# Kernel tuning notes

Measured on AMD Instinct MI355X. Metric: run time of the kernel, lower is better.

## Reference

```python
import jax, jax.numpy as jnp
import numpy as np

N_NODES = 100000
N_EDGES = 1600000
IN_DIM = 256
HID = 32
HEADS = 4
NEG_SLOPE = 0.2


def _seg_softmax(e, seg, n):
    # numerically stable softmax of e [E, H] over segments (destination nodes)
    m = jax.ops.segment_max(e, seg, num_segments=n)
    ex = jnp.exp(e - m[seg])
    s = jax.ops.segment_sum(ex, seg, num_segments=n)
    return ex / (s[seg] + 1e-16)


def _gat_layer(x, W, a_src, a_dst, b, src, dst, n):
    H, D = a_src.shape
    h = (x @ W).reshape(n, H, D)                       # [N, H, D]
    e_src = jnp.sum(h * a_src, axis=-1)                # [N, H]
    e_dst = jnp.sum(h * a_dst, axis=-1)                # [N, H]
    e = jax.nn.leaky_relu(e_src[src] + e_dst[dst], NEG_SLOPE)  # [E, H]
    alpha = _seg_softmax(e, dst, n)                    # [E, H]
    msg = h[src] * alpha[:, :, None]                   # [E, H, D]
    out = jax.ops.segment_sum(msg, dst, num_segments=n)
    return out.reshape(n, H * D) + b


def setup_inputs() -> dict:
    key = jax.random.key(0)
    ks = jax.random.split(key, 20)
    x = jax.random.normal(ks[0], (N_NODES, IN_DIM), dtype=jnp.float32)
    edge_index = jax.random.randint(ks[1], (2, N_EDGES), 0, N_NODES, dtype=jnp.int64)
    s = 0.05
    inp = {"x": x, "edge_index": edge_index}
    inp["W_in"] = jax.random.normal(ks[2], (IN_DIM, HID), dtype=jnp.float32) * s
    inp["b_in"] = jnp.zeros((HID,), dtype=jnp.float32)
    in_dims = [HID, HID * HEADS, HID * HEADS]
    for l in range(3):
        k = jax.random.split(ks[3 + l], 4)
        inp[f"W{l}"] = jax.random.normal(k[0], (in_dims[l], HEADS * HID), dtype=jnp.float32) * s
        inp[f"a_src{l}"] = jax.random.normal(k[1], (HEADS, HID), dtype=jnp.float32) * s
        inp[f"a_dst{l}"] = jax.random.normal(k[2], (HEADS, HID), dtype=jnp.float32) * s
        inp[f"b{l}"] = jnp.zeros((HEADS * HID,), dtype=jnp.float32)
    return inp


def reference(x, edge_index, W_in, b_in,
              W0, a_src0, a_dst0, b0,
              W1, a_src1, a_dst1, b1,
              W2, a_src2, a_dst2, b2):
    n = x.shape[0]
    # PyG GATConv adds self-loops by default
    loops = jnp.arange(n, dtype=edge_index.dtype)
    src = jnp.concatenate([edge_index[0], loops])
    dst = jnp.concatenate([edge_index[1], loops])

    h = jax.nn.relu(x @ W_in + b_in)
    params = [(W0, a_src0, a_dst0, b0), (W1, a_src1, a_dst1, b1), (W2, a_src2, a_dst2, b2)]
    for (W, a_s, a_d, b) in params:
        h = _gat_layer(h, W, a_s, a_d, b, src, dst, n)
        h = jax.nn.elu(h)
        # dropout omitted (eval mode / deterministic reference)
    return h
```

## Files before the change

kernel.cpp:

```cpp
#include <hip/hip_runtime.h>
#include <hip/hip_fp16.h>

#define NN 100000
#define NE 1600000
#define ET (NE + NN)
#define BKW 512
#define NBK ((NN + BKW - 1) / BKW)
#define LCOL_CAP 12288
#define EPB 16384

typedef _Float16 half8_t __attribute__((ext_vector_type(8)));
typedef float f32x4_t __attribute__((ext_vector_type(4)));

__device__ __forceinline__ unsigned enc_f32(float v) {
    unsigned b = __float_as_uint(v);
    return b ^ ((b & 0x80000000u) ? 0xFFFFFFFFu : 0x80000000u);
}
__device__ __forceinline__ float dec_f32(unsigned u) {
    unsigned b = (u & 0x80000000u) ? (u ^ 0x80000000u) : ~u;
    return __uint_as_float(b);
}


__global__ __launch_bounds__(256) void lin_relu2(const float* __restrict__ x,
                                                 const float* __restrict__ W,
                                                 const float* __restrict__ b,
                                                 float* __restrict__ h) {
    __shared__ float Wl[256 * 32];
    int t = threadIdx.x;
    for (int j = 0; j < 8; ++j) {
        int f = t + 256 * j;
        *(float4*)&Wl[f * 4] = *(const float4*)(W + f * 4);
    }
    __syncthreads();

    int row = (blockIdx.x * 256 + t) >> 3;
    int c0  = (t & 7) * 4;
    const float* xr = x + (long long)row * 256;
    float4 acc = {0.f, 0.f, 0.f, 0.f};
    for (int k4 = 0; k4 < 64; ++k4) {
        float4 xv = *(const float4*)(xr + k4 * 4);
        float4 w0 = *(const float4*)&Wl[(k4 * 4 + 0) * 32 + c0];
        float4 w1 = *(const float4*)&Wl[(k4 * 4 + 1) * 32 + c0];
        float4 w2 = *(const float4*)&Wl[(k4 * 4 + 2) * 32 + c0];
        float4 w3 = *(const float4*)&Wl[(k4 * 4 + 3) * 32 + c0];
        acc.x += xv.x * w0.x + xv.y * w1.x + xv.z * w2.x + xv.w * w3.x;
        acc.y += xv.x * w0.y + xv.y * w1.y + xv.z * w2.y + xv.w * w3.y;
        acc.z += xv.x * w0.z + xv.y * w1.z + xv.z * w2.z + xv.w * w3.z;
        acc.w += xv.x * w0.w + xv.y * w1.w + xv.z * w2.w + xv.w * w3.w;
    }
    float4 bv = *(const float4*)(b + c0);
    acc.x = fmaxf(acc.x + bv.x, 0.f);
    acc.y = fmaxf(acc.y + bv.y, 0.f);
    acc.z = fmaxf(acc.z + bv.z, 0.f);
    acc.w = fmaxf(acc.w + bv.w, 0.f);
    *(float4*)(h + (long long)row * 32 + c0) = acc;
}

template<int K>
__global__ __launch_bounds__(256) void gemm_att5(const float* __restrict__ hin,
                                                 const float* __restrict__ W,
                                                 const float* __restrict__ asrc,
                                                 const float* __restrict__ adst,
                                                 __half* __restrict__ hph,
                                                 float* __restrict__ es,
                                                 float* __restrict__ ed,
                                                 unsigned* __restrict__ mxl) {
    __shared__ float hl[64][K + 4];
    __shared__ unsigned lmx[8];
    int t = threadIdx.x;
    int base = blockIdx.x * 64;

    for (int j = 0; j < K / 16; ++j) {
        int f = t + 256 * j;
        int row = f / (K / 4);
        int kq = f % (K / 4);
        int gr = base + row;
        float4 v = {0.f, 0.f, 0.f, 0.f};
        if (gr < NN) v = *(const float4*)(hin + (long long)gr * K + kq * 4);
        *(float4*)&hl[row][kq * 4] = v;
    }
    if (t < 8) lmx[t] = 0u;
    __syncthreads();

    int cg = t & 31, c0 = cg * 4;
    int rq = t >> 5, r0 = rq * 8;
    float4 acc[8];
    #pragma unroll
    for (int i = 0; i < 8; ++i) acc[i] = make_float4(0.f, 0.f, 0.f, 0.f);

    for (int k4 = 0; k4 < K / 4; ++k4) {
        float4 w0 = *(const float4*)(W + (k4 * 4 + 0) * 128 + c0);
        float4 w1 = *(const float4*)(W + (k4 * 4 + 1) * 128 + c0);
        float4 w2 = *(const float4*)(W + (k4 * 4 + 2) * 128 + c0);
        float4 w3 = *(const float4*)(W + (k4 * 4 + 3) * 128 + c0);
        #pragma unroll
        for (int i = 0; i < 8; ++i) {
            float4 hv = *(const float4*)&hl[r0 + i][k4 * 4];
            acc[i].x += hv.x * w0.x + hv.y * w1.x + hv.z * w2.x + hv.w * w3.x;
            acc[i].y += hv.x * w0.y + hv.y * w1.y + hv.z * w2.y + hv.w * w3.y;
            acc[i].z += hv.x * w0.z + hv.y * w1.z + hv.z * w2.z + hv.w * w3.z;
            acc[i].w += hv.x * w0.w + hv.y * w1.w + hv.z * w2.w + hv.w * w3.w;
        }
    }

    int head = cg >> 3;
    int d0 = (cg & 7) * 4;
    float4 as4 = *(const float4*)(asrc + head * 32 + d0);
    float4 ad4 = *(const float4*)(adst + head * 32 + d0);
    float smax = -1e30f, dmax = -1e30f;
    #pragma unroll
    for (int i = 0; i < 8; ++i) {
        int gr = base + r0 + i;
        if (gr >= NN) break;
        __half2 p0 = __floats2half2_rn(acc[i].x, acc[i].y);
        __half2 p1 = __floats2half2_rn(acc[i].z, acc[i].w);
        uint2 pk;
        pk.x = *(unsigned*)&p0;
        pk.y = *(unsigned*)&p1;
        *(uint2*)(hph + (long long)gr * 128 + c0) = pk;
        float ps = acc[i].x * as4.x + acc[i].y * as4.y + acc[i].z * as4.z + acc[i].w * as4.w;
        float pd = acc[i].x * ad4.x + acc[i].y * ad4.y + acc[i].z * ad4.z + acc[i].w * ad4.w;
        for (int off = 1; off < 8; off <<= 1) {
            ps += __shfl_xor(ps, off, 8);
            pd += __shfl_xor(pd, off, 8);
        }
        if ((cg & 7) == 0) {
            es[gr * 4 + head] = ps;
            ed[gr * 4 + head] = pd;
            smax = fmaxf(smax, ps);
            dmax = fmaxf(dmax, pd);
        }
    }
    if ((cg & 7) == 0) {
        atomicMax(&lmx[head], enc_f32(smax));
        atomicMax(&lmx[4 + head], enc_f32(dmax));
    }
    __syncthreads();
    if (t < 8) atomicMax(mxl + t, lmx[t]);
}

__global__ __launch_bounds__(256) void wf_prep(const float* __restrict__ W,
                                               _Float16* __restrict__ Wf) {
    int id = blockIdx.x * 256 + threadIdx.x;
    if (id >= 2048) return;
    int lane = id & 63;
    int q = id >> 6;
    int ks = q & 3;
    int n = q >> 2;
    int col = n * 16 + (lane & 15);
    int k0 = ks * 32 + ((lane >> 4) << 3);
    _Float16 tmp[8];
    #pragma unroll
    for (int j = 0; j < 8; ++j) tmp[j] = (_Float16)W[(k0 + j) * 128 + col];
    *(half8_t*)(Wf + (size_t)id * 8) = *(half8_t*)tmp;
}

__global__ __launch_bounds__(256) void gemm_mfma(const __half* __restrict__ ah,
                                                 const _Float16* __restrict__ Wf,
                                                 const float* __restrict__ asrc,
                                                 const float* __restrict__ adst,
                                                 __half* __restrict__ hph,
                                                 float* __restrict__ es,
                                                 float* __restrict__ ed,
                                                 unsigned* __restrict__ mxl) {
    __shared__ unsigned lmx[8];
    int t = threadIdx.x;
    if (t < 8) lmx[t] = 0u;
    __syncthreads();

    int lane = t & 63, wid = t >> 6;
    int li = lane & 15, lg = lane >> 4;
    int base = blockIdx.x * 128 + wid * 32;
    int r0 = base + li, r1 = r0 + 16;
    long long r0c = min(r0, NN - 1), r1c = min(r1, NN - 1);
    const _Float16* A = (const _Float16*)ah;

    f32x4_t acc[2][8];
    #pragma unroll
    for (int m = 0; m < 2; ++m)
        #pragma unroll
        for (int n = 0; n < 8; ++n) acc[m][n] = (f32x4_t){0.f, 0.f, 0.f, 0.f};

    #pragma unroll
    for (int ks = 0; ks < 4; ++ks) {
        half8_t a0 = *(const half8_t*)(A + r0c * 128 + ks * 32 + lg * 8);
        half8_t a1 = *(const half8_t*)(A + r1c * 128 + ks * 32 + lg * 8);
        #pragma unroll
        for (int n = 0; n < 8; ++n) {
            half8_t b = *(const half8_t*)(Wf + (size_t)((n * 4 + ks) * 64 + lane) * 8);
            acc[0][n] = __builtin_amdgcn_mfma_f32_16x16x32_f16(a0, b, acc[0][n], 0, 0, 0);
            acc[1][n] = __builtin_amdgcn_mfma_f32_16x16x32_f16(a1, b, acc[1][n], 0, 0, 0);
        }
    }

    float as_lo[4], as_hi[4], ad_lo[4], ad_hi[4];
    #pragma unroll
    for (int h = 0; h < 4; ++h) {
        as_lo[h] = asrc[h * 32 + li];
        as_hi[h] = asrc[h * 32 + 16 + li];
        ad_lo[h] = adst[h * 32 + li];
        ad_hi[h] = adst[h * 32 + 16 + li];
    }

    float smax[4] = {-1e30f, -1e30f, -1e30f, -1e30f};
    float dmax[4] = {-1e30f, -1e30f, -1e30f, -1e30f};
    #pragma unroll
    for (int m = 0; m < 2; ++m) {
        #pragma unroll
        for (int r = 0; r < 4; ++r) {
            int gr = base + m * 16 + lg * 4 + r;
            bool valid = gr < NN;
            float ps[4], pd[4];
            #pragma unroll
            for (int h = 0; h < 4; ++h) {
                float va = acc[m][2 * h][r];
                float vb = acc[m][2 * h + 1][r];
                if (valid) {
                    hph[(long long)gr * 128 + h * 32 + li] = __float2half(va);
                    hph[(long long)gr * 128 + h * 32 + 16 + li] = __float2half(vb);
                }
                ps[h] = va * as_lo[h] + vb * as_hi[h];
                pd[h] = va * ad_lo[h] + vb * ad_hi[h];
            }
            #pragma unroll
            for (int off = 1; off < 16; off <<= 1) {
                #pragma unroll
                for (int h = 0; h < 4; ++h) {
                    ps[h] += __shfl_xor(ps[h], off);
                    pd[h] += __shfl_xor(pd[h], off);
                }
            }
            if (li == 0 && valid) {
                #pragma unroll
                for (int h = 0; h < 4; ++h) {
                    es[gr * 4 + h] = ps[h];
                    ed[gr * 4 + h] = pd[h];
                    smax[h] = fmaxf(smax[h], ps[h]);
                    dmax[h] = fmaxf(dmax[h], pd[h]);
                }
            }
        }
    }
    if (li == 0) {
        #pragma unroll
        for (int h = 0; h < 4; ++h) {
            atomicMax(&lmx[h], enc_f32(smax[h]));
            atomicMax(&lmx[4 + h], enc_f32(dmax[h]));
        }
    }
    __syncthreads();
    if (t < 8) atomicMax(mxl + t, lmx[t]);
}


__global__ __launch_bounds__(256) void bucket_hist(const int* __restrict__ ei,
                                                   int* __restrict__ bhist) {
    __shared__ int lh[NBK];
    int t = threadIdx.x;
    for (int i = t; i < NBK; i += 256) lh[i] = 0;
    __syncthreads();
    for (long long e = (long long)blockIdx.x * 256 + t; e < ET; e += (long long)gridDim.x * 256) {
        int dst = (e < NE) ? ei[NE + e] : (int)(e - NE);
        atomicAdd(&lh[dst >> 9], 1);
    }
    __syncthreads();
    for (int i = t; i < NBK; i += 256) if (lh[i]) atomicAdd(&bhist[i], lh[i]);
}

__global__ __launch_bounds__(256) void bucket_scan(const int* __restrict__ bhist,
                                                   int* __restrict__ bbase,
                                                   int* __restrict__ bcur) {
    __shared__ int ls[256];
    int t = threadIdx.x;
    int v = (t < NBK) ? bhist[t] : 0;
    ls[t] = v;
    __syncthreads();
    for (int off = 1; off < 256; off <<= 1) {
        int u = (t >= off) ? ls[t - off] : 0;
        __syncthreads();
        ls[t] += u;
        __syncthreads();
    }
    if (t < NBK) { int b0 = ls[t] - v; bbase[t] = b0; bcur[t] = b0; }
    if (t == 0) bbase[NBK] = ET;
}

__global__ __launch_bounds__(256) void bucket_scatter(const int* __restrict__ ei,
                                                      int* __restrict__ bcur,
                                                      unsigned* __restrict__ brec) {
    __shared__ int lcnt[NBK];
    __shared__ int lbase[NBK];
    int t = threadIdx.x;
    long long e0 = (long long)blockIdx.x * EPB;
    for (int i = t; i < NBK; i += 256) lcnt[i] = 0;
    __syncthreads();
    for (int j = 0; j < EPB / 256; ++j) {
        long long e = e0 + j * 256 + t;
        if (e < ET) {
            int dst = (e < NE) ? ei[NE + e] : (int)(e - NE);
            atomicAdd(&lcnt[dst >> 9], 1);
        }
    }
    __syncthreads();
    for (int i = t; i < NBK; i += 256) {
        int c = lcnt[i];
        lbase[i] = c ? atomicAdd(&bcur[i], c) : 0;
        lcnt[i] = 0;
    }
    __syncthreads();
    for (int j = 0; j < EPB / 256; ++j) {
        long long e = e0 + j * 256 + t;
        if (e < ET) {
            int src, dst;
            if (e < NE) { src = ei[e]; dst = ei[NE + e]; }
            else        { src = dst = (int)(e - NE); }
            int b = dst >> 9;
            int off = atomicAdd(&lcnt[b], 1);
            brec[lbase[b] + off] = ((unsigned)(dst & 511) << 17) | (unsigned)src;
        }
    }
}

__global__ __launch_bounds__(256) void bucket_csr(const unsigned* __restrict__ brec,
                                                  const int* __restrict__ bbase,
                                                  int* __restrict__ row_ptr,
                                                  int* __restrict__ col) {
    __shared__ int ldeg[BKW];
    __shared__ int lrp[BKW + 1];
    __shared__ int lcur[BKW];
    __shared__ int ls[256];
    __shared__ int lcol[LCOL_CAP];
    int t = threadIdx.x, b = blockIdx.x;
    int rbeg = bbase[b], rend = bbase[b + 1];
    int cnt = rend - rbeg;
    for (int i = t; i < BKW; i += 256) ldeg[i] = 0;
    __syncthreads();
    for (int i = t; i < cnt; i += 256) {
        unsigned r = brec[rbeg + i];
        atomicAdd(&ldeg[r >> 17], 1);
    }
    __syncthreads();
    int a0 = ldeg[2 * t], a1 = ldeg[2 * t + 1];
    int pl = a0 + a1;
    ls[t] = pl;
    __syncthreads();
    for (int off = 1; off < 256; off <<= 1) {
        int u = (t >= off) ? ls[t - off] : 0;
        __syncthreads();
        ls[t] += u;
        __syncthreads();
    }
    int eb = ls[t] - pl;
    lrp[2 * t] = eb;
    lrp[2 * t + 1] = eb + a0;
    lcur[2 * t] = eb;
    lcur[2 * t + 1] = eb + a0;
    if (t == 255) lrp[BKW] = ls[255];
    __syncthreads();
    int gn0 = b * BKW;
    int nnb = min(BKW, NN - gn0);
    for (int i = t; i <= nnb; i += 256) row_ptr[gn0 + i] = rbeg + lrp[i];
    for (int i = t; i < cnt; i += 256) {
        unsigned r = brec[rbeg + i];
        int pos = atomicAdd(&lcur[r >> 17], 1);
        lcol[pos] = (int)(r & 0x1FFFFu);
    }
    __syncthreads();
    for (int i = t; i < cnt; i += 256) col[rbeg + i] = lcol[i];
}

__global__ __launch_bounds__(256) void gat_aggregate4(
        const int* __restrict__ row_ptr, const int* __restrict__ col,
        const float* __restrict__ es, const float* __restrict__ ed,
        const unsigned* __restrict__ mx, const __half* __restrict__ hph,
        const float* __restrict__ b, float* __restrict__ outf,
        __half* __restrict__ outh) {
    int tid = blockIdx.x * 256 + threadIdx.x;
    int n = tid >> 4;
    int t = tid & 15;
    if (n >= NN) return;
    int head = t >> 2;
    int beg = row_ptr[n], end = row_ptr[n + 1];

    float Craw = dec_f32(mx[head]) + dec_f32(mx[4 + head]);
    float C = Craw > 0.f ? Craw : 0.2f * Craw;
    float edv = ed[n * 4 + head];

    float acc[8] = {0.f, 0.f, 0.f, 0.f, 0.f, 0.f, 0.f, 0.f};
    float ws = 0.f;
    const __half* hb = hph + (long long)t * 8;

    int i = beg;
    for (; i + 3 < end; i += 4) {
        int s0 = col[i], s1 = col[i + 1], s2 = col[i + 2], s3 = col[i + 3];
        float l0 = es[s0 * 4 + head] + edv;
        float l1 = es[s1 * 4 + head] + edv;
        float l2 = es[s2 * 4 + head] + edv;
        float l3 = es[s3 * 4 + head] + edv;
        uint4 g0 = *(const uint4*)(hb + (long long)s0 * 128);
        uint4 g1 = *(const uint4*)(hb + (long long)s1 * 128);
        uint4 g2 = *(const uint4*)(hb + (long long)s2 * 128);
        uint4 g3 = *(const uint4*)(hb + (long long)s3 * 128);
        l0 = l0 > 0.f ? l0 : 0.2f * l0;
        l1 = l1 > 0.f ? l1 : 0.2f * l1;
        l2 = l2 > 0.f ? l2 : 0.2f * l2;
        l3 = l3 > 0.f ? l3 : 0.2f * l3;
        float w0 = __expf(l0 - C);
        float w1 = __expf(l1 - C);
        float w2 = __expf(l2 - C);
        float w3 = __expf(l3 - C);
        ws += (w0 + w1) + (w2 + w3);
        float2 f;
        f = __half22float2(*(__half2*)&g0.x); acc[0] += w0 * f.x; acc[1] += w0 * f.y;
        f = __half22float2(*(__half2*)&g0.y); acc[2] += w0 * f.x; acc[3] += w0 * f.y;
        f = __half22float2(*(__half2*)&g0.z); acc[4] += w0 * f.x; acc[5] += w0 * f.y;
        f = __half22float2(*(__half2*)&g0.w); acc[6] += w0 * f.x; acc[7] += w0 * f.y;
        f = __half22float2(*(__half2*)&g1.x); acc[0] += w1 * f.x; acc[1] += w1 * f.y;
        f = __half22float2(*(__half2*)&g1.y); acc[2] += w1 * f.x; acc[3] += w1 * f.y;
        f = __half22float2(*(__half2*)&g1.z); acc[4] += w1 * f.x; acc[5] += w1 * f.y;
        f = __half22float2(*(__half2*)&g1.w); acc[6] += w1 * f.x; acc[7] += w1 * f.y;
        f = __half22float2(*(__half2*)&g2.x); acc[0] += w2 * f.x; acc[1] += w2 * f.y;
        f = __half22float2(*(__half2*)&g2.y); acc[2] += w2 * f.x; acc[3] += w2 * f.y;
        f = __half22float2(*(__half2*)&g2.z); acc[4] += w2 * f.x; acc[5] += w2 * f.y;
        f = __half22float2(*(__half2*)&g2.w); acc[6] += w2 * f.x; acc[7] += w2 * f.y;
        f = __half22float2(*(__half2*)&g3.x); acc[0] += w3 * f.x; acc[1] += w3 * f.y;
        f = __half22float2(*(__half2*)&g3.y); acc[2] += w3 * f.x; acc[3] += w3 * f.y;
        f = __half22float2(*(__half2*)&g3.z); acc[4] += w3 * f.x; acc[5] += w3 * f.y;
        f = __half22float2(*(__half2*)&g3.w); acc[6] += w3 * f.x; acc[7] += w3 * f.y;
    }
    for (; i < end; ++i) {
        int s = col[i];
        float lv = es[s * 4 + head] + edv;
        lv = lv > 0.f ? lv : 0.2f * lv;
        float w = __expf(lv - C);
        ws += w;
        uint4 g = *(const uint4*)(hb + (long long)s * 128);
        float2 f;
        f = __half22float2(*(__half2*)&g.x); acc[0] += w * f.x; acc[1] += w * f.y;
        f = __half22float2(*(__half2*)&g.y); acc[2] += w * f.x; acc[3] += w * f.y;
        f = __half22float2(*(__half2*)&g.z); acc[4] += w * f.x; acc[5] += w * f.y;
        f = __half22float2(*(__half2*)&g.w); acc[6] += w * f.x; acc[7] += w * f.y;
    }
    float sv = ws + 1e-16f;
    float vals[8];
    #pragma unroll
    for (int j = 0; j < 8; ++j) {
        float v = acc[j] / sv + b[t * 8 + j];
        vals[j] = v > 0.f ? v : expm1f(v);
    }
    if (outf) {
        float4 v0 = {vals[0], vals[1], vals[2], vals[3]};
        float4 v1 = {vals[4], vals[5], vals[6], vals[7]};
        *(float4*)(outf + (long long)n * 128 + t * 8) = v0;
        *(float4*)(outf + (long long)n * 128 + t * 8 + 4) = v1;
    } else {
        __half o[8];
        #pragma unroll
        for (int j = 0; j < 8; ++j) o[j] = __float2half(vals[j]);
        *(uint4*)(outh + (long long)n * 128 + t * 8) = *(uint4*)o;
    }
}


extern "C" void kernel_launch(void* const* d_in, const int* in_sizes, int n_in,
                              void* d_out, int out_size, void* d_ws, size_t ws_size,
                              hipStream_t stream) {
    const float* x    = (const float*)d_in[0];
    const int*   ei   = (const int*)d_in[1];
    const float* W_in = (const float*)d_in[2];
    const float* b_in = (const float*)d_in[3];
    const float* W[3]  = {(const float*)d_in[4], (const float*)d_in[8],  (const float*)d_in[12]};
    const float* As[3] = {(const float*)d_in[5], (const float*)d_in[9],  (const float*)d_in[13]};
    const float* Ad[3] = {(const float*)d_in[6], (const float*)d_in[10], (const float*)d_in[14]};
    const float* Bs[3] = {(const float*)d_in[7], (const float*)d_in[11], (const float*)d_in[15]};

    float*    h0   = (float*)d_ws;
    __half*   hph  = (__half*)(h0 + (size_t)NN * 32);
    __half*   ah   = hph + (size_t)NN * 128;
    float*    es   = (float*)(ah + (size_t)NN * 128);
    float*    ed   = es + (size_t)NN * 4;
    int*   row_ptr = (int*)(ed + (size_t)NN * 4);
    int*    bhist  = row_ptr + (NN + 1);
    int*    bbase  = bhist + NBK;
    int*    bcur   = bbase + (NBK + 1);
    unsigned* mx   = (unsigned*)(bcur + NBK);
    _Float16* Wf1  = (_Float16*)(mx + 24);
    _Float16* Wf2  = Wf1 + 2048 * 8;
    unsigned* brec = (unsigned*)(Wf2 + 2048 * 8);
    int*    colb   = (int*)(brec + ET);

    hipMemsetAsync(bhist, 0, NBK * sizeof(int), stream);
    hipMemsetAsync(mx, 0, 24 * sizeof(unsigned), stream);
    bucket_hist<<<512, 256, 0, stream>>>(ei, bhist);
    bucket_scan<<<1, 256, 0, stream>>>(bhist, bbase, bcur);
    bucket_scatter<<<(ET + EPB - 1) / EPB, 256, 0, stream>>>(ei, bcur, brec);
    bucket_csr<<<NBK, 256, 0, stream>>>(brec, bbase, row_ptr, colb);

    lin_relu2<<<3125, 256, 0, stream>>>(x, W_in, b_in, h0);
    wf_prep<<<8, 256, 0, stream>>>(W[1], Wf1);
    wf_prep<<<8, 256, 0, stream>>>(W[2], Wf2);

    gemm_att5<32><<<1563, 256, 0, stream>>>(h0, W[0], As[0], Ad[0], hph, es, ed, mx);
    gat_aggregate4<<<6250, 256, 0, stream>>>(row_ptr, colb, es, ed, mx, hph, Bs[0],
                                             nullptr, ah);
    gemm_mfma<<<782, 256, 0, stream>>>(ah, Wf1, As[1], Ad[1], hph, es, ed, mx + 8);
    gat_aggregate4<<<6250, 256, 0, stream>>>(row_ptr, colb, es, ed, mx + 8, hph, Bs[1],
                                             nullptr, ah);
    gemm_mfma<<<782, 256, 0, stream>>>(ah, Wf2, As[2], Ad[2], hph, es, ed, mx + 16);
    gat_aggregate4<<<6250, 256, 0, stream>>>(row_ptr, colb, es, ed, mx + 16, hph, Bs[2],
                                             (float*)d_out, nullptr);
}
```

Baseline: 499.3 us.

## Sort nodes by degree and share attention weights across lanes in aggregation

Adds a counting sort of destination nodes by in-degree (histogram, scan, scatter), so each wavefront handles nodes of similar degree and divergence in the edge loop shrinks. The aggregation kernel now walks nodes through that permutation, aligns the column index to a multiple of 4 so it can use int4 loads, and has each of the 4 lanes in a head compute one edge's exp weight, then broadcast it with shuffles instead of every lane computing all four. The cost is three small extra kernels and an indirection per node. Output writes become scattered in node order, and the peeling loop adds some extra scalar work.

```diff
diff --git a/kernel.cpp b/kernel.cpp
--- a/kernel.cpp
+++ b/kernel.cpp
@@ -370,17 +370,52 @@
     for (int i = t; i < cnt; i += 256) col[rbeg + i] = lcol[i];
 }
 
-__global__ __launch_bounds__(256) void gat_aggregate4(
+__global__ __launch_bounds__(256) void deg_hist(const int* __restrict__ row_ptr,
+                                                int* __restrict__ dh) {
+    int n = blockIdx.x * 256 + threadIdx.x;
+    if (n >= NN) return;
+    int d = row_ptr[n + 1] - row_ptr[n];
+    atomicAdd(dh + min(d, 63), 1);
+}
+__global__ __launch_bounds__(64) void deg_scan(const int* __restrict__ dh,
+                                               int* __restrict__ dcur) {
+    __shared__ int ls[64];
+    int t = threadIdx.x;
+    int v = dh[t];
+    ls[t] = v;
+    __syncthreads();
+    for (int off = 1; off < 64; off <<= 1) {
+        int u = (t >= off) ? ls[t - off] : 0;
+        __syncthreads();
+        ls[t] += u;
+        __syncthreads();
+    }
+    dcur[t] = ls[t] - v;
+}
+__global__ __launch_bounds__(256) void deg_scatter(const int* __restrict__ row_ptr,
+                                                   int* __restrict__ dcur,
+                                                   int* __restrict__ nperm) {
+    int n = blockIdx.x * 256 + threadIdx.x;
+    if (n >= NN) return;
+    int d = row_ptr[n + 1] - row_ptr[n];
+    int p = atomicAdd(dcur + min(d, 63), 1);
+    nperm[p] = n;
+}
+
+__global__ __launch_bounds__(256) void gat_aggregate5(
+        const int* __restrict__ nperm,
         const int* __restrict__ row_ptr, const int* __restrict__ col,
         const float* __restrict__ es, const float* __restrict__ ed,
         const unsigned* __restrict__ mx, const __half* __restrict__ hph,
         const float* __restrict__ b, float* __restrict__ outf,
         __half* __restrict__ outh) {
     int tid = blockIdx.x * 256 + threadIdx.x;
-    int n = tid >> 4;
+    int g = tid >> 4;
     int t = tid & 15;
-    if (n >= NN) return;
+    if (g >= NN) return;
+    int n = nperm[g];
     int head = t >> 2;
+    int j = t & 3;
     int beg = row_ptr[n], end = row_ptr[n + 1];
 
     float Craw = dec_f32(mx[head]) + dec_f32(mx[4 + head]);
@@ -392,24 +427,34 @@
     const __half* hb = hph + (long long)t * 8;
 
     int i = beg;
+    int alim = (beg + 3) & ~3;
+    for (; i < end && i < alim; ++i) {
+        int s = col[i];
+        float lv = es[s * 4 + head] + edv;
+        lv = lv > 0.f ? lv : 0.2f * lv;
+        float w = __expf(lv - C);
+        ws += w;
+        uint4 gv = *(const uint4*)(hb + (long long)s * 128);
+        float2 f;
+        f = __half22float2(*(__half2*)&gv.x); acc[0] += w * f.x; acc[1] += w * f.y;
+        f = __half22float2(*(__half2*)&gv.y); acc[2] += w * f.x; acc[3] += w * f.y;
+        f = __half22float2(*(__half2*)&gv.z); acc[4] += w * f.x; acc[5] += w * f.y;
+        f = __half22float2(*(__half2*)&gv.w); acc[6] += w * f.x; acc[7] += w * f.y;
+    }
     for (; i + 3 < end; i += 4) {
-        int s0 = col[i], s1 = col[i + 1], s2 = col[i + 2], s3 = col[i + 3];
-        float l0 = es[s0 * 4 + head] + edv;
-        float l1 = es[s1 * 4 + head] + edv;
-        float l2 = es[s2 * 4 + head] + edv;
-        float l3 = es[s3 * 4 + head] + edv;
-        uint4 g0 = *(const uint4*)(hb + (long long)s0 * 128);
-        uint4 g1 = *(const uint4*)(hb + (long long)s1 * 128);
-        uint4 g2 = *(const uint4*)(hb + (long long)s2 * 128);
-        uint4 g3 = *(const uint4*)(hb + (long long)s3 * 128);
-        l0 = l0 > 0.f ? l0 : 0.2f * l0;
-        l1 = l1 > 0.f ? l1 : 0.2f * l1;
-        l2 = l2 > 0.f ? l2 : 0.2f * l2;
-        l3 = l3 > 0.f ? l3 : 0.2f * l3;
-        float w0 = __expf(l0 - C);
-        float w1 = __expf(l1 - C);
-        float w2 = __expf(l2 - C);
-        float w3 = __expf(l3 - C);
+        int4 s4 = *(const int4*)(col + i);
+        int sj = (j == 0) ? s4.x : (j == 1) ? s4.y : (j == 2) ? s4.z : s4.w;
+        float lv = es[sj * 4 + head] + edv;
+        lv = lv > 0.f ? lv : 0.2f * lv;
+        float wj = __expf(lv - C);
+        float w0 = __shfl(wj, 0, 4);
+        float w1 = __shfl(wj, 1, 4);
+        float w2 = __shfl(wj, 2, 4);
+        float w3 = __shfl(wj, 3, 4);
+        uint4 g0 = *(const uint4*)(hb + (long long)s4.x * 128);
+        uint4 g1 = *(const uint4*)(hb + (long long)s4.y * 128);
+        uint4 g2 = *(const uint4*)(hb + (long long)s4.z * 128);
+        uint4 g3 = *(const uint4*)(hb + (long long)s4.w * 128);
         ws += (w0 + w1) + (w2 + w3);
         float2 f;
         f = __half22float2(*(__half2*)&g0.x); acc[0] += w0 * f.x; acc[1] += w0 * f.y;
@@ -435,19 +480,20 @@
         lv = lv > 0.f ? lv : 0.2f * lv;
         float w = __expf(lv - C);
         ws += w;
-        uint4 g = *(const uint4*)(hb + (long long)s * 128);
+        uint4 gv = *(const uint4*)(hb + (long long)s * 128);
         float2 f;
-        f = __half22float2(*(__half2*)&g.x); acc[0] += w * f.x; acc[1] += w * f.y;
-        f = __half22float2(*(__half2*)&g.y); acc[2] += w * f.x; acc[3] += w * f.y;
-        f = __half22float2(*(__half2*)&g.z); acc[4] += w * f.x; acc[5] += w * f.y;
-        f = __half22float2(*(__half2*)&g.w); acc[6] += w * f.x; acc[7] += w * f.y;
-    }
+        f = __half22float2(*(__half2*)&gv.x); acc[0] += w * f.x; acc[1] += w * f.y;
+        f = __half22float2(*(__half2*)&gv.y); acc[2] += w * f.x; acc[3] += w * f.y;
+        f = __half22float2(*(__half2*)&gv.z); acc[4] += w * f.x; acc[5] += w * f.y;
+        f = __half22float2(*(__half2*)&gv.w); acc[6] += w * f.x; acc[7] += w * f.y;
+    }
+
     float sv = ws + 1e-16f;
     float vals[8];
     #pragma unroll
-    for (int j = 0; j < 8; ++j) {
-        float v = acc[j] / sv + b[t * 8 + j];
-        vals[j] = v > 0.f ? v : expm1f(v);
+    for (int k = 0; k < 8; ++k) {
+        float v = acc[k] / sv + b[t * 8 + k];
+        vals[k] = v > 0.f ? v : expm1f(v);
     }
     if (outf) {
         float4 v0 = {vals[0], vals[1], vals[2], vals[3]};
@@ -457,7 +503,7 @@
     } else {
         __half o[8];
         #pragma unroll
-        for (int j = 0; j < 8; ++j) o[j] = __float2half(vals[j]);
+        for (int k = 0; k < 8; ++k) o[k] = __float2half(vals[k]);
         *(uint4*)(outh + (long long)n * 128 + t * 8) = *(uint4*)o;
     }
 }
@@ -485,29 +531,36 @@
     int*    bbase  = bhist + NBK;
     int*    bcur   = bbase + (NBK + 1);
     unsigned* mx   = (unsigned*)(bcur + NBK);
-    _Float16* Wf1  = (_Float16*)(mx + 24);
+    int*    dh     = (int*)(mx + 24);
+    int*    dcur   = dh + 64;
+    int*    nperm  = dcur + 64;
+    _Float16* Wf1  = (_Float16*)(nperm + NN);
     _Float16* Wf2  = Wf1 + 2048 * 8;
     unsigned* brec = (unsigned*)(Wf2 + 2048 * 8);
     int*    colb   = (int*)(brec + ET);
 
     hipMemsetAsync(bhist, 0, NBK * sizeof(int), stream);
     hipMemsetAsync(mx, 0, 24 * sizeof(unsigned), stream);
+    hipMemsetAsync(dh, 0, 64 * sizeof(int), stream);
     bucket_hist<<<512, 256, 0, stream>>>(ei, bhist);
     bucket_scan<<<1, 256, 0, stream>>>(bhist, bbase, bcur);
     bucket_scatter<<<(ET + EPB - 1) / EPB, 256, 0, stream>>>(ei, bcur, brec);
     bucket_csr<<<NBK, 256, 0, stream>>>(brec, bbase, row_ptr, colb);
+    deg_hist<<<(NN + 255) / 256, 256, 0, stream>>>(row_ptr, dh);
+    deg_scan<<<1, 64, 0, stream>>>(dh, dcur);
+    deg_scatter<<<(NN + 255) / 256, 256, 0, stream>>>(row_ptr, dcur, nperm);
 
     lin_relu2<<<3125, 256, 0, stream>>>(x, W_in, b_in, h0);
     wf_prep<<<8, 256, 0, stream>>>(W[1], Wf1);
     wf_prep<<<8, 256, 0, stream>>>(W[2], Wf2);
 
     gemm_att5<32><<<1563, 256, 0, stream>>>(h0, W[0], As[0], Ad[0], hph, es, ed, mx);
-    gat_aggregate4<<<6250, 256, 0, stream>>>(row_ptr, colb, es, ed, mx, hph, Bs[0],
+    gat_aggregate5<<<6250, 256, 0, stream>>>(nperm, row_ptr, colb, es, ed, mx, hph, Bs[0],
                                              nullptr, ah);
     gemm_mfma<<<782, 256, 0, stream>>>(ah, Wf1, As[1], Ad[1], hph, es, ed, mx + 8);
-    gat_aggregate4<<<6250, 256, 0, stream>>>(row_ptr, colb, es, ed, mx + 8, hph, Bs[1],
+    gat_aggregate5<<<6250, 256, 0, stream>>>(nperm, row_ptr, colb, es, ed, mx + 8, hph, Bs[1],
                                              nullptr, ah);
     gemm_mfma<<<782, 256, 0, stream>>>(ah, Wf2, As[2], Ad[2], hph, es, ed, mx + 16);
-    gat_aggregate4<<<6250, 256, 0, stream>>>(row_ptr, colb, es, ed, mx + 16, hph, Bs[2],
+    gat_aggregate5<<<6250, 256, 0, stream>>>(nperm, row_ptr, colb, es, ed, mx + 16, hph, Bs[2],
                                              (float*)d_out, nullptr);
 }
```

After: 1.136 ms. 2.27x slower.
